# Kernel optimization log

Measured on AMD Instinct MI355X. Metric: run time of the kernel, lower is better.

Reference implementation:

```python
import jax, jax.numpy as jnp
import numpy as np

B, D, H, C, T = 65536, 512, 256, 100, 10
EPS = 0.01  # halt_epsilon


def setup_inputs() -> dict:
    key = jax.random.key(0)
    ks = jax.random.split(key, 10)
    sD = 1.0 / np.sqrt(D)
    sH = 1.0 / np.sqrt(H)
    return {
        "x": jax.random.normal(ks[0], (B, D), dtype=jnp.float32),
        # GRUCell params (PyTorch layout: rows chunked as [r; z; n])
        "W_ih": jax.random.uniform(ks[1], (3 * H, D), minval=-sD, maxval=sD, dtype=jnp.float32),
        "W_hh": jax.random.uniform(ks[2], (3 * H, H), minval=-sH, maxval=sH, dtype=jnp.float32),
        "b_ih": jax.random.uniform(ks[3], (3 * H,), minval=-sH, maxval=sH, dtype=jnp.float32),
        "b_hh": jax.random.uniform(ks[4], (3 * H,), minval=-sH, maxval=sH, dtype=jnp.float32),
        # halting unit
        "W_halt": jax.random.uniform(ks[5], (1, H), minval=-sH, maxval=sH, dtype=jnp.float32),
        "b_halt": jax.random.uniform(ks[6], (1,), minval=-sH, maxval=sH, dtype=jnp.float32),
        # readout
        "W_ro": jax.random.uniform(ks[7], (C, H), minval=-sH, maxval=sH, dtype=jnp.float32),
        "b_ro": jax.random.uniform(ks[8], (C,), minval=-sH, maxval=sH, dtype=jnp.float32),
    }


def _act_forward(x, W_ih, W_hh, b_ih, b_hh, W_halt, b_halt, W_ro, b_ro):
    dt = x.dtype
    thresh = jnp.asarray(1.0 - EPS, dt)
    # x is static across ponder steps -> precompute input projection once
    x_proj = x @ W_ih.T + b_ih                       # [B, 3H]
    xr, xz, xn = jnp.split(x_proj, 3, axis=-1)

    def step(carry, _):
        h, cum, rem, nup, acc = carry
        h_proj = h @ W_hh.T + b_hh                   # [B, 3H]
        hr, hz, hn = jnp.split(h_proj, 3, axis=-1)
        r = jax.nn.sigmoid(xr + hr)
        z = jax.nn.sigmoid(xz + hz)
        n = jnp.tanh(xn + r * hn)
        h_new = (1.0 - z) * n + z * h                # GRUCell update
        halt = jax.nn.sigmoid(h_new @ W_halt.T + b_halt)[:, 0]  # [B]
        logits_t = h_new @ W_ro.T + b_ro             # [B, C]
        still = (cum < thresh).astype(dt)
        new_halt = halt * still
        would = (cum + new_halt > thresh).astype(dt)
        remainder = (1.0 - cum) * would * still
        step_w = new_halt * (1.0 - would) + remainder
        cum2 = cum + step_w
        acc2 = acc + step_w[:, None] * h_new
        return (h_new, cum2, rem + remainder, nup + still, acc2), (h_new, halt, logits_t)

    zB = jnp.zeros((x.shape[0],), dt)
    init = (jnp.zeros((x.shape[0], W_hh.shape[1]), dt), zB, zB, zB,
            jnp.zeros((x.shape[0], W_hh.shape[1]), dt))
    (h, cum, remainders, n_updates, acc), (h_seq, halt_seq, logits_seq) = jax.lax.scan(
        step, init, None, length=T)
    logits = acc @ W_ro.T + b_ro                     # [B, C]
    ponder_cost = n_updates.mean() + remainders.mean()
    # scan stacks on axis 0 (time) -> move to dim 1 as torch.stack(dim=1)
    h_seq = jnp.swapaxes(h_seq, 0, 1)                # [B, T, H]
    halt_seq = jnp.swapaxes(halt_seq, 0, 1)          # [B, T]
    logits_seq = jnp.swapaxes(logits_seq, 0, 1)      # [B, T, C]
    return logits, ponder_cost, n_updates, h_seq, halt_seq, logits_seq


def reference(x, W_ih, W_hh, b_ih, b_hh, W_halt, b_halt, W_ro, b_ro):
    return _act_forward(x, W_ih, W_hh, b_ih, b_hh, W_halt, b_halt, W_ro, b_ro)
```

## Files before the change

kernel.cpp:

```cpp
#include <hip/hip_runtime.h>
#include <cmath>


namespace {
constexpr int B = 65536, D = 512, H = 256, C = 100, T = 10;

constexpr long OUT_LOGITS = 0;
constexpr long OUT_PONDER = (long)B * C;
constexpr long OUT_NUP    = OUT_PONDER + 1;
constexpr long OUT_HSEQ   = OUT_NUP + B;
constexpr long OUT_HALT   = OUT_HSEQ + (long)B * T * H;
constexpr long OUT_LSEQ   = OUT_HALT + (long)B * T;
constexpr long OUT_H16    = (OUT_LSEQ + 3) & ~3L;

constexpr long NIH  = 768L * D;
constexpr long NHH  = 768L * H;
constexpr long NAUG = 112L * H;

constexpr long WS_XP   = 0;
constexpr long WS_W16  = WS_XP + (long)B * 768;
constexpr long W_HALV  = 2 * (NIH + NHH + NAUG);
constexpr long WS_HL   = WS_W16 + (W_HALV + 1) / 2;
constexpr long WS_HP4  = WS_HL + (long)B * T;
constexpr long WS_NUPB = WS_HP4 + 4L * B * T;
constexpr long WS_REMB = WS_NUPB + B;

constexpr float SC = 256.f;
constexpr float SB = 1.f / 65536.f;
}

typedef __attribute__((ext_vector_type(8))) _Float16 h8;
typedef __attribute__((ext_vector_type(4))) _Float16 h4;
typedef __attribute__((ext_vector_type(4))) float f4;

#define MFMA16(A, Bo, Cc) __builtin_amdgcn_mfma_f32_16x16x32_f16(A, Bo, Cc, 0, 0, 0)
#define PROD3(a, Ah, Al, Bh, Bl)                                               \
  a = MFMA16(Al, Bh, a);                                                       \
  a = MFMA16(Ah, Bl, a);                                                       \
  a = MFMA16(Ah, Bh, a);

__device__ __forceinline__ float sigmoidf_(float x) {
  if (x >= 0.f) { return 1.f / (1.f + expf(-x)); }
  float e = expf(x);
  return e / (1.f + e);
}

__device__ __forceinline__ void gload_lds16(const _Float16* g, _Float16* l) {
  __builtin_amdgcn_global_load_lds(
      (const __attribute__((address_space(1))) unsigned int*)g,
      (__attribute__((address_space(3))) unsigned int*)l, 16, 0, 0);
}

__global__ void k_prep(const float* __restrict__ wih_s, const float* __restrict__ whh_s,
                       const float* __restrict__ wro, const float* __restrict__ whalt,
                       _Float16* __restrict__ wr) {
  long idx = (long)blockIdx.x * 256 + threadIdx.x;
  if (idx < NIH) {
    float xs = wih_s[idx] * SC;
    _Float16 h = (_Float16)xs;
    _Float16 l = (_Float16)(xs - (float)h);
    wr[idx] = h; wr[NIH + idx] = l;
  }
  if (idx < NHH) {
    float xs = whh_s[idx] * SC;
    _Float16 h = (_Float16)xs;
    _Float16 l = (_Float16)(xs - (float)h);
    long b = 2 * NIH;
    wr[b + idx] = h; wr[b + NHH + idx] = l;
  }
  if (idx < NAUG) {
    int row = (int)(idx >> 8), k = (int)(idx & 255);
    float x = (row < C) ? wro[row * 256 + k] : ((row == C) ? whalt[k] : 0.f);
    float xs = x * SC;
    _Float16 h = (_Float16)xs;
    _Float16 l = (_Float16)(xs - (float)h);
    long b = 2 * (NIH + NHH);
    wr[b + idx] = h; wr[b + NAUG + idx] = l;
  }
}

__device__ __forceinline__ void stageA16(const float* __restrict__ src,
                                         _Float16* As0, _Float16* As1,
                                         int o) {
#pragma unroll
  for (int i = 0; i < 4; ++i) {
    float4 v = ((const float4*)src)[i];
    float vv[4] = {v.x, v.y, v.z, v.w};
    h4 hh, ll;
#pragma unroll
    for (int c = 0; c < 4; ++c) {
      float sv = vv[c] * SC;
      _Float16 h = (_Float16)sv;
      hh[c] = h;
      ll[c] = (_Float16)(sv - (float)h);
    }
    *(h4*)&As0[o + i * 4] = hh;
    *(h4*)&As1[o + i * 4] = ll;
  }
}

__global__ __launch_bounds__(256, 2) void k_xproj(
    const float* __restrict__ x, const _Float16* __restrict__ wih,
    const float* __restrict__ b_ih, float* __restrict__ xp) {
  __shared__ __align__(16) _Float16 As0[128 * 40], As1[128 * 40];
  __shared__ __align__(16) _Float16 Bs[2][192 * 32];
  const int tid = threadIdx.x;
  const int w = tid >> 6, l = tid & 63;
  const int lr = l & 15, lq = l >> 4;
  const int bid = blockIdx.x;
  const int gid = (bid & 7) * 256 + (bid >> 3);
  const int c0 = (gid & 3) * 64;
  const int rb = (gid >> 2) * 128;

  f4 acc[8][3];
#pragma unroll
  for (int i = 0; i < 8; ++i)
#pragma unroll
    for (int g = 0; g < 3; ++g) acc[i][g] = (f4)0.f;

  for (int kc = 0; kc < 16; ++kc) {
    const int k0 = kc * 32;
    __syncthreads();
    {
      const int row = tid >> 1, kk0 = (tid & 1) * 16;
      stageA16(x + (long)(rb + row) * D + k0 + kk0, As0, As1, row * 40 + kk0);
    }
#pragma unroll
    for (int j = 0; j < 6; ++j) {
      int chunk = w * 6 + j;
      int plane = chunk / 12;
      int rem = chunk - plane * 12;
      int scol = rem * 16 + (l >> 2);
      int kq = l & 3;
      int gcol = (scol >> 6) * 256 + c0 + (scol & 63);
      gload_lds16(wih + (long)plane * NIH + (long)gcol * D + k0 + kq * 8,
                  &Bs[plane][rem * 512]);
    }
    __syncthreads();
    h8 Bh[3], Bl[3];
#pragma unroll
    for (int g = 0; g < 3; ++g) {
      Bh[g] = *(const h8*)&Bs[0][(g * 64 + w * 16 + lr) * 32 + lq * 8];
      Bl[g] = *(const h8*)&Bs[1][(g * 64 + w * 16 + lr) * 32 + lq * 8];
    }
#pragma unroll
    for (int i = 0; i < 8; ++i) {
      h8 Ah = *(const h8*)&As0[(i * 16 + lr) * 40 + lq * 8];
      h8 Al = *(const h8*)&As1[(i * 16 + lr) * 40 + lq * 8];
#pragma unroll
      for (int g = 0; g < 3; ++g) { PROD3(acc[i][g], Ah, Al, Bh[g], Bl[g]); }
    }
  }
  const int ch = c0 + w * 16 + lr;
  float bi[3] = {b_ih[ch], b_ih[256 + ch], b_ih[512 + ch]};
#pragma unroll
  for (int i = 0; i < 8; ++i)
#pragma unroll
    for (int g = 0; g < 3; ++g)
#pragma unroll
      for (int reg = 0; reg < 4; ++reg) {
        long row = rb + i * 16 + lq * 4 + reg;
        xp[row * 768 + g * 256 + ch] = fmaf(acc[i][g][reg], SB, bi[g]);
      }
}

__global__ __launch_bounds__(256, 2) void k_gru(
    const _Float16* __restrict__ whh, const float* __restrict__ xp,
    const float* __restrict__ b_hh, const float* __restrict__ w_halt,
    float* __restrict__ out, _Float16* __restrict__ h16,
    float* __restrict__ hp4, int t) {
  __shared__ __align__(16) _Float16 As[2][128 * 32];
  __shared__ __align__(16) _Float16 Bs[2][192 * 32];
  __shared__ float lds_hp[128][4];
  const int tid = threadIdx.x;
  const int w = tid >> 6, l = tid & 63;
  const int lr = l & 15, lq = l >> 4;
  const int bid = blockIdx.x;
  const int gid = (bid & 7) * 256 + (bid >> 3);
  const int strip = gid & 3;
  const int c0 = strip * 64;
  const int rb = (gid >> 2) * 128;
  const long tilebase = (long)(rb >> 7) * 65536;

  f4 acc[8][3];
#pragma unroll
  for (int i = 0; i < 8; ++i)
#pragma unroll
    for (int g = 0; g < 3; ++g) acc[i][g] = (f4)0.f;

  if (t > 0) {
    for (int kc = 0; kc < 8; ++kc) {
      const int k0 = kc * 32;
      __syncthreads();
#pragma unroll
      for (int j = 0; j < 4; ++j) {
        int c8 = w * 4 + j;
        int plane = c8 >> 3;
        int c = c8 & 7;
        gload_lds16(h16 + tilebase + (long)kc * 8192 + plane * 4096 + c * 512 + l * 8,
                    &As[plane][c * 512]);
      }
#pragma unroll
      for (int j = 0; j < 6; ++j) {
        int chunk = w * 6 + j;
        int plane = chunk / 12;
        int rem = chunk - plane * 12;
        int scol = rem * 16 + (l >> 2);
        int kq = l & 3;
        int gcol = (scol >> 6) * 256 + c0 + (scol & 63);
        gload_lds16(whh + (long)plane * NHH + (long)gcol * H + k0 + kq * 8,
                    &Bs[plane][rem * 512]);
      }
      __syncthreads();
      h8 Bh[3], Bl[3];
#pragma unroll
      for (int g = 0; g < 3; ++g) {
        Bh[g] = *(const h8*)&Bs[0][(g * 64 + w * 16 + lr) * 32 + lq * 8];
        Bl[g] = *(const h8*)&Bs[1][(g * 64 + w * 16 + lr) * 32 + lq * 8];
      }
#pragma unroll
      for (int i = 0; i < 8; ++i) {
        h8 Ah = *(const h8*)&As[0][(i * 16 + lr) * 32 + lq * 8];
        h8 Al = *(const h8*)&As[1][(i * 16 + lr) * 32 + lq * 8];
#pragma unroll
        for (int g = 0; g < 3; ++g) { PROD3(acc[i][g], Ah, Al, Bh[g], Bl[g]); }
      }
    }
  }

  const int ch = c0 + w * 16 + lr;
  const float bhr = b_hh[ch], bhz = b_hh[256 + ch], bhn = b_hh[512 + ch];
  const float whv = w_halt[ch];
  const long h16c = tilebase + (long)(ch >> 5) * 8192 + (ch & 31);
#pragma unroll
  for (int i = 0; i < 8; ++i)
#pragma unroll
    for (int reg = 0; reg < 4; ++reg) {
      const int rloc = i * 16 + lq * 4 + reg;
      const long row = rb + rloc;
      float xr = xp[row * 768 + ch];
      float xz = xp[row * 768 + 256 + ch];
      float xn = xp[row * 768 + 512 + ch];
      float ho = (t > 0) ? out[OUT_HSEQ + row * (T * H) + (long)(t - 1) * H + ch] : 0.f;
      float rr = sigmoidf_(xr + fmaf(acc[i][0][reg], SB, bhr));
      float zz = sigmoidf_(xz + fmaf(acc[i][1][reg], SB, bhz));
      float nn = tanhf(xn + rr * fmaf(acc[i][2][reg], SB, bhn));
      float hv = (1.f - zz) * nn + zz * ho;
      out[OUT_HSEQ + row * (T * H) + (long)t * H + ch] = hv;
      float sv = hv * SC;
      _Float16 hi = (_Float16)sv;
      _Float16 lo = (_Float16)(sv - (float)hi);
      h16[h16c + (long)rloc * 32] = hi;
      h16[h16c + 4096 + (long)rloc * 32] = lo;
      float p = hv * whv;
#pragma unroll
      for (int m = 1; m < 16; m <<= 1) p += __shfl_xor(p, m, 64);
      if (lr == 0) lds_hp[rloc][w] = p;
    }
  __syncthreads();
  if (tid < 128)
    hp4[((long)t * 4 + strip) * B + rb + tid] =
        ((lds_hp[tid][0] + lds_hp[tid][1]) + (lds_hp[tid][2] + lds_hp[tid][3]));
}

__global__ __launch_bounds__(256, 4) void k_lseq(
    const float* __restrict__ hseq, const _Float16* __restrict__ waug,
    const float* __restrict__ b_ro, float* __restrict__ lseq) {
  __shared__ __align__(16) _Float16 As0[128 * 40];
  __shared__ __align__(16) _Float16 Bs[112 * 32];
  const int tid = threadIdx.x;
  const int w = tid >> 6, l = tid & 63;
  const int lr = l & 15, lq = l >> 4;
  const long mb = (long)blockIdx.x * 128;

  f4 acc[2][7];
#pragma unroll
  for (int i = 0; i < 2; ++i)
#pragma unroll
    for (int j = 0; j < 7; ++j) acc[i][j] = (f4)0.f;

  for (int kc = 0; kc < 8; ++kc) {
    const int k0 = kc * 32;
    __syncthreads();
    {
      const int row = tid >> 1, kk0 = (tid & 1) * 16;
      const float* src = hseq + (mb + row) * H + k0 + kk0;
      const int o = row * 40 + kk0;
#pragma unroll
      for (int i = 0; i < 4; ++i) {
        float4 v = ((const float4*)src)[i];
        h4 hh;
        hh[0] = (_Float16)(v.x * SC); hh[1] = (_Float16)(v.y * SC);
        hh[2] = (_Float16)(v.z * SC); hh[3] = (_Float16)(v.w * SC);
        *(h4*)&As0[o + i * 4] = hh;
      }
    }
#pragma unroll
    for (int j = 0; j < 2; ++j) {
      int chunk = w + j * 4;
      if (chunk < 7) {
        int scol = chunk * 16 + (l >> 2);
        int kq = l & 3;
        gload_lds16(waug + (long)scol * H + k0 + kq * 8, &Bs[chunk * 512]);
      }
    }
    __syncthreads();
    h8 Af[2];
#pragma unroll
    for (int i = 0; i < 2; ++i)
      Af[i] = *(const h8*)&As0[(w * 32 + i * 16 + lr) * 40 + lq * 8];
#pragma unroll
    for (int j = 0; j < 7; ++j) {
      h8 Bf = *(const h8*)&Bs[(j * 16 + lr) * 32 + lq * 8];
#pragma unroll
      for (int i = 0; i < 2; ++i) acc[i][j] = MFMA16(Af[i], Bf, acc[i][j]);
    }
  }
#pragma unroll
  for (int j = 0; j < 7; ++j) {
    const int col = j * 16 + lr;
    if (col < C) {
      const float br = b_ro[col];
#pragma unroll
      for (int i = 0; i < 2; ++i)
#pragma unroll
        for (int reg = 0; reg < 4; ++reg) {
          long m = mb + w * 32 + i * 16 + lq * 4 + reg;
          lseq[m * C + col] = fmaf(acc[i][j][reg], SB, br);
        }
    }
  }
}

__global__ void k_act(const float* __restrict__ hp4, const float* __restrict__ b_halt,
                      float* __restrict__ out, float* __restrict__ swb,
                      float* __restrict__ nupb, float* __restrict__ remb) {
  const long b = (long)blockIdx.x * 256 + threadIdx.x;
  const float bh = b_halt[0];
  float cum = 0.f, rem = 0.f, nu = 0.f;
#pragma unroll
  for (int t = 0; t < T; ++t) {
    float v = bh + hp4[((long)t * 4 + 0) * B + b] + hp4[((long)t * 4 + 1) * B + b] +
              hp4[((long)t * 4 + 2) * B + b] + hp4[((long)t * 4 + 3) * B + b];
    float halt = sigmoidf_(v);
    out[OUT_HALT + b * T + t] = halt;
    float still = (cum < 0.99f) ? 1.f : 0.f;
    float nh = halt * still;
    float would = ((cum + nh) > 0.99f) ? 1.f : 0.f;
    float rema = (1.f - cum) * would * still;
    float swv = nh * (1.f - would) + rema;
    cum += swv; rem += rema; nu += still;
    swb[b * T + t] = swv;
  }
  nupb[b] = nu; remb[b] = rem;
}

__global__ void k_logits(const float* __restrict__ lseq, const float* __restrict__ swb,
                         const float* __restrict__ b_ro, const float* __restrict__ nupb,
                         float* __restrict__ out) {
  const long b = blockIdx.x;
  const int tid = threadIdx.x;
  if (tid < C) {
    float br = b_ro[tid];
    float s = br;
#pragma unroll
    for (int t = 0; t < T; ++t) {
      float sw = swb[b * T + t];
      s = fmaf(sw, lseq[(b * T + t) * C + tid] - br, s);
    }
    out[OUT_LOGITS + b * C + tid] = s;
  } else if (tid == C) {
    out[OUT_NUP + b] = nupb[b];
  }
}

__global__ void k_ponder(const float* __restrict__ nupb, const float* __restrict__ remb,
                         float* __restrict__ out) {
  __shared__ float sm[4];
  float s = 0.f;
  for (int i = threadIdx.x; i < B; i += 256) s += nupb[i] + remb[i];
#pragma unroll
  for (int m = 1; m < 64; m <<= 1) s += __shfl_xor(s, m, 64);
  int w = threadIdx.x >> 6;
  if ((threadIdx.x & 63) == 0) sm[w] = s;
  __syncthreads();
  if (threadIdx.x == 0)
    out[OUT_PONDER] = (sm[0] + sm[1] + sm[2] + sm[3]) * (1.f / (float)B);
}

extern "C" void kernel_launch(void* const* d_in, const int* in_sizes, int n_in,
                              void* d_out, int out_size, void* d_ws, size_t ws_size,
                              hipStream_t stream) {
  const float* x      = (const float*)d_in[0];
  const float* W_ih   = (const float*)d_in[1];
  const float* W_hh   = (const float*)d_in[2];
  const float* b_ih   = (const float*)d_in[3];
  const float* b_hh   = (const float*)d_in[4];
  const float* W_halt = (const float*)d_in[5];
  const float* b_halt = (const float*)d_in[6];
  const float* W_ro   = (const float*)d_in[7];
  const float* b_ro   = (const float*)d_in[8];
  float* out = (float*)d_out;
  float* ws  = (float*)d_ws;

  float* xp        = ws + WS_XP;
  _Float16* w16    = (_Float16*)(ws + WS_W16);
  _Float16* wih16  = w16;
  _Float16* whh16  = w16 + 2 * NIH;
  _Float16* waug16 = w16 + 2 * (NIH + NHH);
  float* swb  = ws + WS_HL;
  float* hp4  = ws + WS_HP4;
  float* nupb = ws + WS_NUPB;
  float* remb = ws + WS_REMB;
  _Float16* h16 = (_Float16*)(out + OUT_H16);

  k_prep<<<(int)((NIH + 255) / 256), 256, 0, stream>>>(W_ih, W_hh, W_ro, W_halt, w16);
  k_xproj<<<2048, 256, 0, stream>>>(x, wih16, b_ih, xp);
  for (int t = 0; t < T; ++t)
    k_gru<<<2048, 256, 0, stream>>>(whh16, xp, b_hh, W_halt, out, h16, hp4, t);
  k_lseq<<<(B * T) / 128, 256, 0, stream>>>(out + OUT_HSEQ, waug16, b_ro, out + OUT_LSEQ);
  k_act<<<B / 256, 256, 0, stream>>>(hp4, b_halt, out, swb, nupb, remb);
  k_logits<<<B, 128, 0, stream>>>(out + OUT_LSEQ, swb, b_ro, nupb, out);
  k_ponder<<<1, 256, 0, stream>>>(nupb, remb, out);
}
```

Baseline: 2.311 ms.

## Keep per-step fp16 hidden states in workspace and feed readout GEMM directly

The fp16 hi/lo hidden-state buffer moves from the output tail into the workspace, with one slab per timestep instead of a single overwritten slab. The readout kernel now loads the pre-tiled fp16 hi plane straight into LDS with async global-to-LDS copies, replacing reads of fp32 h_seq that were converted on the fly. Its grid is remapped to (t, batch tile) and writes logits_seq at the matching strided position. Launch bounds for the xproj and GRU kernels are raised to 3 blocks per CU to increase occupancy. This needs a much larger workspace (about 2*B*H*T halves), and the higher occupancy target may force register spills.

```diff
diff --git a/kernel.cpp b/kernel.cpp
--- a/kernel.cpp
+++ b/kernel.cpp
@@ -11,7 +11,6 @@
 constexpr long OUT_HSEQ   = OUT_NUP + B;
 constexpr long OUT_HALT   = OUT_HSEQ + (long)B * T * H;
 constexpr long OUT_LSEQ   = OUT_HALT + (long)B * T;
-constexpr long OUT_H16    = (OUT_LSEQ + 3) & ~3L;
 
 constexpr long NIH  = 768L * D;
 constexpr long NHH  = 768L * H;
@@ -24,6 +23,8 @@
 constexpr long WS_HP4  = WS_HL + (long)B * T;
 constexpr long WS_NUPB = WS_HP4 + 4L * B * T;
 constexpr long WS_REMB = WS_NUPB + B;
+constexpr long WS_H16  = WS_REMB + B;
+constexpr long H16_PER_T = 512L * 65536;
 
 constexpr float SC = 256.f;
 constexpr float SB = 1.f / 65536.f;
@@ -99,7 +100,7 @@
   }
 }
 
-__global__ __launch_bounds__(256, 2) void k_xproj(
+__global__ __launch_bounds__(256, 3) void k_xproj(
     const float* __restrict__ x, const _Float16* __restrict__ wih,
     const float* __restrict__ b_ih, float* __restrict__ xp) {
   __shared__ __align__(16) _Float16 As0[128 * 40], As1[128 * 40];
@@ -164,7 +165,7 @@
       }
 }
 
-__global__ __launch_bounds__(256, 2) void k_gru(
+__global__ __launch_bounds__(256, 3) void k_gru(
     const _Float16* __restrict__ whh, const float* __restrict__ xp,
     const float* __restrict__ b_hh, const float* __restrict__ w_halt,
     float* __restrict__ out, _Float16* __restrict__ h16,
@@ -189,6 +190,7 @@
     for (int g = 0; g < 3; ++g) acc[i][g] = (f4)0.f;
 
   if (t > 0) {
+    const _Float16* h16r = h16 + (long)(t - 1) * H16_PER_T + tilebase;
     for (int kc = 0; kc < 8; ++kc) {
       const int k0 = kc * 32;
       __syncthreads();
@@ -197,7 +199,7 @@
         int c8 = w * 4 + j;
         int plane = c8 >> 3;
         int c = c8 & 7;
-        gload_lds16(h16 + tilebase + (long)kc * 8192 + plane * 4096 + c * 512 + l * 8,
+        gload_lds16(h16r + (long)kc * 8192 + plane * 4096 + c * 512 + l * 8,
                     &As[plane][c * 512]);
       }
 #pragma unroll
@@ -231,7 +233,7 @@
   const int ch = c0 + w * 16 + lr;
   const float bhr = b_hh[ch], bhz = b_hh[256 + ch], bhn = b_hh[512 + ch];
   const float whv = w_halt[ch];
-  const long h16c = tilebase + (long)(ch >> 5) * 8192 + (ch & 31);
+  const long h16c = (long)t * H16_PER_T + tilebase + (long)(ch >> 5) * 8192 + (ch & 31);
 #pragma unroll
   for (int i = 0; i < 8; ++i)
 #pragma unroll
@@ -264,14 +266,16 @@
 }
 
 __global__ __launch_bounds__(256, 4) void k_lseq(
-    const float* __restrict__ hseq, const _Float16* __restrict__ waug,
+    const _Float16* __restrict__ h16, const _Float16* __restrict__ waug,
     const float* __restrict__ b_ro, float* __restrict__ lseq) {
-  __shared__ __align__(16) _Float16 As0[128 * 40];
+  __shared__ __align__(16) _Float16 As[128 * 32];
   __shared__ __align__(16) _Float16 Bs[112 * 32];
   const int tid = threadIdx.x;
   const int w = tid >> 6, l = tid & 63;
   const int lr = l & 15, lq = l >> 4;
-  const long mb = (long)blockIdx.x * 128;
+  const int t = blockIdx.x >> 9;
+  const int btile = blockIdx.x & 511;
+  const _Float16* h16r = h16 + (long)t * H16_PER_T + (long)btile * 65536;
 
   f4 acc[2][7];
 #pragma unroll
@@ -282,18 +286,10 @@
   for (int kc = 0; kc < 8; ++kc) {
     const int k0 = kc * 32;
     __syncthreads();
-    {
-      const int row = tid >> 1, kk0 = (tid & 1) * 16;
-      const float* src = hseq + (mb + row) * H + k0 + kk0;
-      const int o = row * 40 + kk0;
-#pragma unroll
-      for (int i = 0; i < 4; ++i) {
-        float4 v = ((const float4*)src)[i];
-        h4 hh;
-        hh[0] = (_Float16)(v.x * SC); hh[1] = (_Float16)(v.y * SC);
-        hh[2] = (_Float16)(v.z * SC); hh[3] = (_Float16)(v.w * SC);
-        *(h4*)&As0[o + i * 4] = hh;
-      }
+#pragma unroll
+    for (int j = 0; j < 2; ++j) {
+      int c = w * 2 + j;
+      gload_lds16(h16r + (long)kc * 8192 + c * 512 + l * 8, &As[c * 512]);
     }
 #pragma unroll
     for (int j = 0; j < 2; ++j) {
@@ -308,7 +304,7 @@
     h8 Af[2];
 #pragma unroll
     for (int i = 0; i < 2; ++i)
-      Af[i] = *(const h8*)&As0[(w * 32 + i * 16 + lr) * 40 + lq * 8];
+      Af[i] = *(const h8*)&As[(w * 32 + i * 16 + lr) * 32 + lq * 8];
 #pragma unroll
     for (int j = 0; j < 7; ++j) {
       h8 Bf = *(const h8*)&Bs[(j * 16 + lr) * 32 + lq * 8];
@@ -325,8 +321,8 @@
       for (int i = 0; i < 2; ++i)
 #pragma unroll
         for (int reg = 0; reg < 4; ++reg) {
-          long m = mb + w * 32 + i * 16 + lq * 4 + reg;
-          lseq[m * C + col] = fmaf(acc[i][j][reg], SB, br);
+          long b = (long)btile * 128 + w * 32 + i * 16 + lq * 4 + reg;
+          lseq[(b * T + t) * C + col] = fmaf(acc[i][j][reg], SB, br);
         }
     }
   }
@@ -412,13 +408,13 @@
   float* hp4  = ws + WS_HP4;
   float* nupb = ws + WS_NUPB;
   float* remb = ws + WS_REMB;
-  _Float16* h16 = (_Float16*)(out + OUT_H16);
+  _Float16* h16 = (_Float16*)(ws + WS_H16);
 
   k_prep<<<(int)((NIH + 255) / 256), 256, 0, stream>>>(W_ih, W_hh, W_ro, W_halt, w16);
   k_xproj<<<2048, 256, 0, stream>>>(x, wih16, b_ih, xp);
   for (int t = 0; t < T; ++t)
     k_gru<<<2048, 256, 0, stream>>>(whh16, xp, b_hh, W_halt, out, h16, hp4, t);
-  k_lseq<<<(B * T) / 128, 256, 0, stream>>>(out + OUT_HSEQ, waug16, b_ro, out + OUT_LSEQ);
+  k_lseq<<<512 * T, 256, 0, stream>>>(h16, waug16, b_ro, out + OUT_LSEQ);
   k_act<<<B / 256, 256, 0, stream>>>(hp4, b_halt, out, swb, nupb, remb);
   k_logits<<<B, 128, 0, stream>>>(out + OUT_LSEQ, swb, b_ro, nupb, out);
   k_ponder<<<1, 256, 0, stream>>>(nupb, remb, out);
```

New measurement: 2.239 ms. -3.1%, faster.
